# Kernel optimization log

Hardware: AMD Instinct MI355X
Metric: run time of the kernel (lower is better)

Reference implementation:

```python
import jax, jax.numpy as jnp
import numpy as np

B, T, E = 1024, 168, 8      # batch, input_len, encoder_input_size
D = 4                        # decoder_input_size
H = 512                      # lstm_num_hidden
O = 24                       # output_len


def setup_inputs() -> dict:
    key = jax.random.key(0)
    ks = jax.random.split(key, 9)
    sc = 1.0 / np.sqrt(H)
    p = lambda k, shape: (jax.random.uniform(k, shape, jnp.float32) * 2 - 1) * sc
    return {
        "x": jax.random.normal(ks[0], (B, T, E), jnp.float32),
        "W_ih_enc": p(ks[1], (4 * H, E)),
        "W_hh_enc": p(ks[2], (4 * H, H)),
        "b_enc":    p(ks[3], (4 * H,)),   # = b_ih + b_hh combined (same math)
        "W_ih_dec": p(ks[4], (4 * H, D)),
        "W_hh_dec": p(ks[5], (4 * H, H)),
        "b_dec":    p(ks[6], (4 * H,)),
        "W_fc":     p(ks[7], (D, H)),
        "b_fc":     p(ks[8], (D,)),
    }


def _lstm_cell(x, h, c, Wih, Whh, b):
    # PyTorch gate order: i, f, g, o
    gates = x @ Wih.T + h @ Whh.T + b            # [B, 4H]
    i, f, g, o = jnp.split(gates, 4, axis=-1)
    c = jax.nn.sigmoid(f) * c + jax.nn.sigmoid(i) * jnp.tanh(g)
    h = jax.nn.sigmoid(o) * jnp.tanh(c)
    return h, c


def reference(x, W_ih_enc, W_hh_enc, b_enc, W_ih_dec, W_hh_dec, b_dec, W_fc, b_fc):
    Bn = x.shape[0]
    Hn = W_hh_enc.shape[1]
    Dn = W_ih_dec.shape[1]
    h0 = jnp.zeros((Bn, Hn), x.dtype)

    # ---- encoder LSTM over input_len steps; keep only final (h, c) ----
    def enc_step(carry, xt):  # xt: [B, E]
        h, c = carry
        h, c = _lstm_cell(xt, h, c, W_ih_enc, W_hh_enc, b_enc)
        return (h, c), None
    (h, c), _ = jax.lax.scan(enc_step, (h0, h0), jnp.swapaxes(x, 0, 1))

    xt0 = x[:, -1, -Dn:]  # [B, D]

    def dec_step(carry, _):
        h, c, xt = carry
        h, c = _lstm_cell(xt, h, c, W_ih_dec, W_hh_dec, b_dec)
        y = h @ W_fc.T + b_fc          # [B, D]  (fc: hidden -> decoder_input)
        return (h, c, y), y[:, -1]     # emit last feature (target)

    _, ys = jax.lax.scan(dec_step, (h, c, xt0), None, length=O)  # [O, B]
    return jnp.swapaxes(ys, 0, 1)[..., None]  # [B, O, 1]
```

## Files before the change

kernel.cpp:

```cpp
#include <hip/hip_runtime.h>

#define Bn 1024
#define Tn 168
#define En 8
#define Hn 512
#define Dn 4
#define On 24
#define G4 2048
#define HB (Bn*Hn)

typedef short v8s __attribute__((ext_vector_type(8)));
typedef float v4f __attribute__((ext_vector_type(4)));

__device__ __forceinline__ unsigned short f2bf(float f) {
  union { float f; unsigned u; } v; v.f = f;
  return (unsigned short)((v.u + 0x7fffu + ((v.u >> 16) & 1u)) >> 16);
}
__device__ __forceinline__ float bf2f(unsigned short s) {
  union { unsigned u; float f; } v; v.u = ((unsigned)s) << 16; return v.f;
}
__device__ __forceinline__ float sigm(float x) { return 1.f / (1.f + __expf(-x)); }
__device__ __forceinline__ float tanh_(float x) { return 1.f - 2.f / (__expf(2.f * x) + 1.f); }

__device__ __forceinline__ void st_short_coh(unsigned short* p, unsigned short v) {
  unsigned int vv = v;
  asm volatile("global_store_short %0, %1, off sc0 sc1" :: "v"(p), "v"(vv) : "memory");
}
__device__ __forceinline__ void st_dword_coh(unsigned* p, unsigned v) {
  asm volatile("global_store_dword %0, %1, off sc0 sc1" :: "v"(p), "v"(v) : "memory");
}
__device__ __forceinline__ unsigned ld_u_coh(const unsigned* p) {
  unsigned v;
  asm volatile("global_load_dword %0, %1, off sc0 sc1\n\ts_waitcnt vmcnt(0)"
               : "=v"(v) : "v"(p) : "memory");
  return v;
}
__device__ __forceinline__ float ld_f_coh(const float* p) {
  float v;
  asm volatile("global_load_dword %0, %1, off sc0 sc1\n\ts_waitcnt vmcnt(0)"
               : "=v"(v) : "v"(p) : "memory");
  return v;
}
#define LDC(dst, p) \
  asm volatile("global_load_dwordx4 %0, %1, off sc0 sc1" : "=&v"(dst) : "v"(p))
#define WAITV(N) do { \
  asm volatile("s_waitcnt vmcnt(" #N ")" ::: "memory"); \
  __builtin_amdgcn_sched_barrier(0); } while (0)


__global__ void setup_weights(const float* __restrict__ whh_enc,
                              const float* __restrict__ whh_dec,
                              const float* __restrict__ wih_dec,
                              const float* __restrict__ wfc,
                              unsigned short* __restrict__ whh_bf,
                              unsigned short* __restrict__ weff_bf) {
  int idx = blockIdx.x * 256 + threadIdx.x;
  if (idx >= G4 * Hn) return;
  int r = idx >> 9, c = idx & 511;
  whh_bf[idx] = f2bf(whh_enc[idx]);
  float a = whh_dec[idx];
#pragma unroll
  for (int d = 0; d < 4; d++) a += wih_dec[r * 4 + d] * wfc[d * Hn + c];
  weff_bf[idx] = f2bf(a);
}

__global__ void setup_misc(const float* __restrict__ b_dec,
                           const float* __restrict__ wih_dec,
                           const float* __restrict__ b_fc,
                           float* __restrict__ beff,
                           float* __restrict__ out,
                           unsigned int* __restrict__ flags,
                           float* __restrict__ dpart) {
  int idx = blockIdx.x * 256 + threadIdx.x;
  if (idx < Bn * On) out[idx] = 0.f;
  if (idx < G4) {
    float a = b_dec[idx];
#pragma unroll
    for (int d = 0; d < 4; d++) a += wih_dec[idx * 4 + d] * b_fc[d];
    beff[idx] = a;
  }
  if (idx < 256 * 64) flags[idx] = 0u;
  if (idx < 16 * 64 * 4) dpart[idx] = 0.f;
}


__global__ void __launch_bounds__(256, 1) lstm_main(
    const float* __restrict__ x,
    const float* __restrict__ wih_enc,
    const float* __restrict__ b_enc,
    const float* __restrict__ wih_dec,
    const float* __restrict__ wfc,
    const float* __restrict__ bfc,
    const unsigned short* __restrict__ whh_bf,
    const unsigned short* __restrict__ weff_bf,
    const float* __restrict__ beff,
    unsigned short* __restrict__ hbuf,
    unsigned short* __restrict__ lbuf,
    float* __restrict__ out,
    unsigned int* __restrict__ flags,
    float* __restrict__ dpart) {
  __shared__ __align__(16) unsigned short wlds[128 * 512];
  __shared__ float xw[128][8];
  __shared__ float xwd[128][4];
  __shared__ float biasl[128];
  __shared__ float wfcs[4][32];
  __shared__ float xs[4][16][8];
  __shared__ float dl0[64][4];
  __shared__ float bfc3s;
  __shared__ unsigned scnt;

  const int tid = threadIdx.x;
  const int w = tid >> 6;
  const int lane = tid & 63;
  const int cidx = lane & 15;
  const int kb = lane >> 4;
  const int sw = cidx & 7;
  const int g = blockIdx.x & 15;
  const int jj = blockIdx.x >> 4;
  const int bb = g * 64;
  unsigned* myflag = flags + (((g << 4) + jj) << 6);
  const unsigned* fpoll = flags + (((g << 4) + (lane & 15)) << 6);

  {
    if (tid == 0) scnt = 0u;
    float4* wq4 = (float4*)wlds;
    for (int i = tid; i < 128 * 64; i += 256) {
      int rl = i >> 6, ch = i & 63;
      int gr = (rl >> 5) * 512 + jj * 32 + (rl & 31);
      wq4[rl * 64 + (ch ^ (rl & 7))] = *(const float4*)(whh_bf + (size_t)gr * Hn + ch * 8);
    }
    for (int i = tid; i < 128 * 8; i += 256) {
      int rl = i >> 3, e = i & 7;
      int gr = (rl >> 5) * 512 + jj * 32 + (rl & 31);
      xw[rl][e] = wih_enc[gr * En + e];
    }
    for (int i = tid; i < 128 * 4; i += 256) {
      int rl = i >> 2, d = i & 3;
      int gr = (rl >> 5) * 512 + jj * 32 + (rl & 31);
      xwd[rl][d] = wih_dec[gr * Dn + d];
    }
    for (int i = tid; i < 128; i += 256) {
      int gr = (i >> 5) * 512 + jj * 32 + (i & 31);
      biasl[i] = b_enc[gr];
    }
    if (tid < 128) wfcs[tid >> 5][tid & 31] = wfc[(tid >> 5) * Hn + jj * 32 + (tid & 31)];
    if (tid == 0) bfc3s = bfc[3];
    for (int i = tid; i < 64 * 32; i += 256) {
      int m = bb + (i >> 5), j = jj * 32 + (i & 31);
      st_short_coh(hbuf + (size_t)m * Hn + j, 0);
      st_short_coh(lbuf + (size_t)m * Hn + j, 0);
    }
  }
  asm volatile("s_waitcnt vmcnt(0)" ::: "memory");
  __syncthreads();
  if (tid == 0) st_dword_coh(myflag, 1u);

  float cst[2][4];
#pragma unroll
  for (int a = 0; a < 2; a++)
#pragma unroll
    for (int r = 0; r < 4; r++) cst[a][r] = 0.f;

  const v8s* wq = (const v8s*)wlds;
  const int abase = (bb + w * 16 + cidx) * Hn + kb * 8;

#define POLL(TGT) do { \
    int guard = 0; \
    while (true) { \
      unsigned fv = ld_u_coh(fpoll); \
      if (__ballot(fv < (unsigned)(TGT)) == 0ull) break; \
      __builtin_amdgcn_s_sleep(1); \
      if (++guard > (1 << 21)) break; \
    } } while (0)

#define ISSUE(AH, AL, K0) \
  _Pragma("unroll") for (int q = 0; q < 4; q++) { \
    LDC(AH[q], (const v8s*)(hsrc + abase + (K0 + q) * 32)); \
    LDC(AL[q], (const v8s*)(lsrc + abase + (K0 + q) * 32)); }

#define MMC(AH, AL, K0) \
  _Pragma("unroll") for (int q = 0; q < 4; q++) \
    _Pragma("unroll") for (int nt = 0; nt < 8; nt++) { \
      v8s bfr = wq[(nt * 16 + cidx) * 64 + ((((K0 + q) * 4) + kb) ^ sw)]; \
      acc[nt] = __builtin_amdgcn_mfma_f32_16x16x32_bf16(AH[q], bfr, acc[nt], 0, 0, 0); \
      acc[nt] = __builtin_amdgcn_mfma_f32_16x16x32_bf16(AL[q], bfr, acc[nt], 0, 0, 0); }

#define HMATMUL(CUR) do { \
    const unsigned short* hsrc = hbuf + (size_t)(CUR) * HB; \
    const unsigned short* lsrc = lbuf + (size_t)(CUR) * HB; \
    v8s a0h[4], a0l[4], a1h[4], a1l[4]; \
    ISSUE(a0h, a0l, 0) ISSUE(a1h, a1l, 4) \
    WAITV(8); MMC(a0h, a0l, 0) \
    ISSUE(a0h, a0l, 8) \
    WAITV(8); MMC(a1h, a1l, 4) \
    ISSUE(a1h, a1l, 12) \
    WAITV(8); MMC(a0h, a0l, 8) \
    WAITV(0); MMC(a1h, a1l, 12) \
  } while (0)

  for (int t = 0; t < Tn; t++) {
    const int cur = t & 1, nxt = cur ^ 1;
    {
      int row = lane >> 2, p2 = lane & 3;
      const float* xp = x + (size_t)(bb + w * 16 + row) * (Tn * En) + t * En + p2 * 2;
      float2 xv = *(const float2*)xp;
      xs[w][row][p2 * 2] = xv.x;
      xs[w][row][p2 * 2 + 1] = xv.y;
      asm volatile("s_waitcnt lgkmcnt(0)" ::: "memory");
    }
    v4f acc[8];
#pragma unroll
    for (int nt = 0; nt < 8; nt++) {
      const int rl = nt * 16 + cidx;
      const float bv = biasl[rl];
#pragma unroll
      for (int r = 0; r < 4; r++) {
        float a = bv;
#pragma unroll
        for (int e = 0; e < 8; e++) a += xs[w][kb * 4 + r][e] * xw[rl][e];
        acc[nt][r] = a;
      }
    }
    POLL(t + 1);
    HMATMUL(cur);
    unsigned short* hdst = hbuf + (size_t)nxt * HB;
    unsigned short* ldst = lbuf + (size_t)nxt * HB;
#pragma unroll
    for (int r = 0; r < 4; r++) {
      float hv[2];
#pragma unroll
      for (int th = 0; th < 2; th++) {
        float iv = acc[0 + th][r], fv = acc[2 + th][r];
        float gv = acc[4 + th][r], ov = acc[6 + th][r];
        float cn = sigm(fv) * cst[th][r] + sigm(iv) * tanh_(gv);
        float hn = sigm(ov) * tanh_(cn);
        cst[th][r] = cn;
        hv[th] = hn;
        const int m = bb + w * 16 + kb * 4 + r;
        const int j = jj * 32 + th * 16 + cidx;
        unsigned short hh = f2bf(hn);
        st_short_coh(hdst + (size_t)m * Hn + j, hh);
        st_short_coh(ldst + (size_t)m * Hn + j, f2bf(hn - bf2f(hh)));
      }
      if (t == Tn - 1) {
#pragma unroll
        for (int d = 0; d < 4; d++) {
          float s = hv[0] * wfcs[d][cidx] + hv[1] * wfcs[d][16 + cidx];
          s += __shfl_xor(s, 1, 64); s += __shfl_xor(s, 2, 64);
          s += __shfl_xor(s, 4, 64); s += __shfl_xor(s, 8, 64);
          if (cidx == 0)
            atomicAdd(dpart + ((g * 64 + w * 16 + kb * 4 + r) * 4 + d), s);
        }
      }
    }
    asm volatile("s_waitcnt vmcnt(0)" ::: "memory");
    if (lane == 0) {
      unsigned old = atomicAdd(&scnt, 1u);
      if ((old & 3u) == 3u) st_dword_coh(myflag, (unsigned)(t + 2));
    }
  }

  __syncthreads();
  {
    float4* wq4 = (float4*)wlds;
    for (int i = tid; i < 128 * 64; i += 256) {
      int rl = i >> 6, ch = i & 63;
      int gr = (rl >> 5) * 512 + jj * 32 + (rl & 31);
      wq4[rl * 64 + (ch ^ (rl & 7))] = *(const float4*)(weff_bf + (size_t)gr * Hn + ch * 8);
    }
    for (int i = tid; i < 128; i += 256) {
      int gr = (i >> 5) * 512 + jj * 32 + (i & 31);
      biasl[i] = beff[gr];
    }
  }
  __syncthreads();

  for (int k = 0; k < On; k++) {
    const int T = Tn + k;
    const int cur = k & 1, nxt = cur ^ 1;
    POLL(T + 1);
    if (k == 0) {
      int row = tid >> 2, d = tid & 3;
      float pv = ld_f_coh(dpart + ((g * 64 + row) * 4 + d));
      float xv = x[(size_t)(bb + row) * (Tn * En) + 167 * En + 4 + d];
      dl0[row][d] = xv - (pv + bfc[d]);
      __syncthreads();
    }
    v4f acc[8];
#pragma unroll
    for (int nt = 0; nt < 8; nt++) {
      const int rl = nt * 16 + cidx;
      const float bv = biasl[rl];
#pragma unroll
      for (int r = 0; r < 4; r++) {
        float a = bv;
        if (k == 0) {
#pragma unroll
          for (int d2 = 0; d2 < 4; d2++)
            a += dl0[w * 16 + kb * 4 + r][d2] * xwd[rl][d2];
        }
        acc[nt][r] = a;
      }
    }
    HMATMUL(cur);
    unsigned short* hdst = hbuf + (size_t)nxt * HB;
    unsigned short* ldst = lbuf + (size_t)nxt * HB;
#pragma unroll
    for (int r = 0; r < 4; r++) {
      float hv[2];
#pragma unroll
      for (int th = 0; th < 2; th++) {
        float iv = acc[0 + th][r], fv = acc[2 + th][r];
        float gv = acc[4 + th][r], ov = acc[6 + th][r];
        float cn = sigm(fv) * cst[th][r] + sigm(iv) * tanh_(gv);
        float hn = sigm(ov) * tanh_(cn);
        cst[th][r] = cn;
        hv[th] = hn;
        const int m = bb + w * 16 + kb * 4 + r;
        const int j = jj * 32 + th * 16 + cidx;
        unsigned short hh = f2bf(hn);
        st_short_coh(hdst + (size_t)m * Hn + j, hh);
        st_short_coh(ldst + (size_t)m * Hn + j, f2bf(hn - bf2f(hh)));
      }
      float p = hv[0] * wfcs[3][cidx] + hv[1] * wfcs[3][16 + cidx];
      p += __shfl_xor(p, 1, 64); p += __shfl_xor(p, 2, 64);
      p += __shfl_xor(p, 4, 64); p += __shfl_xor(p, 8, 64);
      if (cidx == 0) {
        const int m = bb + w * 16 + kb * 4 + r;
        float pp = p + (jj == 0 ? bfc3s : 0.f);
        atomicAdd(out + (size_t)m * On + k, pp);
      }
    }
    asm volatile("s_waitcnt vmcnt(0)" ::: "memory");
    if (lane == 0) {
      unsigned old = atomicAdd(&scnt, 1u);
      if ((old & 3u) == 3u) st_dword_coh(myflag, (unsigned)(T + 2));
    }
  }
}

extern "C" void kernel_launch(void* const* d_in, const int* in_sizes, int n_in,
                              void* d_out, int out_size, void* d_ws, size_t ws_size,
                              hipStream_t stream) {
  const float* x = (const float*)d_in[0];
  const float* wih_enc = (const float*)d_in[1];
  const float* whh_enc = (const float*)d_in[2];
  const float* b_enc = (const float*)d_in[3];
  const float* wih_dec = (const float*)d_in[4];
  const float* whh_dec = (const float*)d_in[5];
  const float* b_dec = (const float*)d_in[6];
  const float* wfc = (const float*)d_in[7];
  const float* bfc = (const float*)d_in[8];

  char* ws = (char*)d_ws;
  unsigned short* whh_bf = (unsigned short*)ws;
  unsigned short* weff_bf = (unsigned short*)(ws + (2u << 20));
  unsigned short* hbuf = (unsigned short*)(ws + (4u << 20));
  unsigned short* lbuf = (unsigned short*)(ws + (6u << 20));
  float* beff = (float*)(ws + (8u << 20));
  unsigned int* flags = (unsigned int*)(ws + (8u << 20) + 8192);
  float* dpart = (float*)(ws + (8u << 20) + 8192 + 65536);
  float* out = (float*)d_out;

  setup_weights<<<(G4 * Hn) / 256, 256, 0, stream>>>(whh_enc, whh_dec, wih_dec, wfc,
                                                     whh_bf, weff_bf);
  setup_misc<<<(Bn * On) / 256, 256, 0, stream>>>(b_dec, wih_dec, bfc, beff, out,
                                                  flags, dpart);
  lstm_main<<<256, 256, 0, stream>>>(x, wih_enc, b_enc, wih_dec, wfc, bfc,
                                     whh_bf, weff_bf, beff, hbuf, lbuf, out,
                                     flags, dpart);
}
```

Baseline: 1.522 ms.

## Use XCD-local cache scope for hidden-state exchange when group shares an XCD

Each block reads the XCC_ID hardware register and publishes it. After the first flag barrier, every block checks whether all 16 blocks of its batch group run on the same XCD. If they do, the recurrent h/l buffers are stored without sc0/sc1 and loaded with sc0 only, so the exchange goes through the shared L2 instead of system-coherent memory. The sc1 variants stay as a fallback, and the encoder and decoder steps are turned into macros templated on that choice. This targets the latency of the per-step cross-block hidden-state exchange. It depends on blocks with the same blockIdx mod 8 being placed on one XCD, and the two copies of the step code increase code size.

```diff
diff --git a/kernel.cpp b/kernel.cpp
--- a/kernel.cpp
+++ b/kernel.cpp
@@ -12,6 +12,8 @@
 typedef short v8s __attribute__((ext_vector_type(8)));
 typedef float v4f __attribute__((ext_vector_type(4)));
 
+#define CAT2(a, b) a##b
+
 __device__ __forceinline__ unsigned short f2bf(float f) {
   union { float f; unsigned u; } v; v.f = f;
   return (unsigned short)((v.u + 0x7fffu + ((v.u >> 16) & 1u)) >> 16);
@@ -22,27 +24,18 @@
 __device__ __forceinline__ float sigm(float x) { return 1.f / (1.f + __expf(-x)); }
 __device__ __forceinline__ float tanh_(float x) { return 1.f - 2.f / (__expf(2.f * x) + 1.f); }
 
-__device__ __forceinline__ void st_short_coh(unsigned short* p, unsigned short v) {
-  unsigned int vv = v;
-  asm volatile("global_store_short %0, %1, off sc0 sc1" :: "v"(p), "v"(vv) : "memory");
-}
-__device__ __forceinline__ void st_dword_coh(unsigned* p, unsigned v) {
-  asm volatile("global_store_dword %0, %1, off sc0 sc1" :: "v"(p), "v"(v) : "memory");
-}
-__device__ __forceinline__ unsigned ld_u_coh(const unsigned* p) {
-  unsigned v;
-  asm volatile("global_load_dword %0, %1, off sc0 sc1\n\ts_waitcnt vmcnt(0)"
-               : "=v"(v) : "v"(p) : "memory");
-  return v;
-}
-__device__ __forceinline__ float ld_f_coh(const float* p) {
-  float v;
-  asm volatile("global_load_dword %0, %1, off sc0 sc1\n\ts_waitcnt vmcnt(0)"
-               : "=v"(v) : "v"(p) : "memory");
-  return v;
-}
-#define LDC(dst, p) \
-  asm volatile("global_load_dwordx4 %0, %1, off sc0 sc1" : "=&v"(dst) : "v"(p))
+#define STFLAG(p, v) do { unsigned __vv = (v); \
+  asm volatile("global_store_dword %0, %1, off sc0 sc1" :: "v"(p), "v"(__vv) : "memory"); } while (0)
+#define LDFLAG(r, p) asm volatile("global_load_dword %0, %1, off sc0 sc1\n\ts_waitcnt vmcnt(0)" \
+  : "=v"(r) : "v"(p) : "memory")
+
+#define STH_0(p, v) do { unsigned __vv = (v); \
+  asm volatile("global_store_short %0, %1, off" :: "v"(p), "v"(__vv) : "memory"); } while (0)
+#define STH_1(p, v) do { unsigned __vv = (v); \
+  asm volatile("global_store_short %0, %1, off sc0 sc1" :: "v"(p), "v"(__vv) : "memory"); } while (0)
+#define LDC_0(dst, p) asm volatile("global_load_dwordx4 %0, %1, off sc0" : "=&v"(dst) : "v"(p))
+#define LDC_1(dst, p) asm volatile("global_load_dwordx4 %0, %1, off sc0 sc1" : "=&v"(dst) : "v"(p))
+
 #define WAITV(N) do { \
   asm volatile("s_waitcnt vmcnt(" #N ")" ::: "memory"); \
   __builtin_amdgcn_sched_barrier(0); } while (0)
@@ -98,6 +91,7 @@
     unsigned short* __restrict__ lbuf,
     float* __restrict__ out,
     unsigned int* __restrict__ flags,
+    unsigned int* __restrict__ xcds,
     float* __restrict__ dpart) {
   __shared__ __align__(16) unsigned short wlds[128 * 512];
   __shared__ float xw[128][8];
@@ -121,6 +115,9 @@
   unsigned* myflag = flags + (((g << 4) + jj) << 6);
   const unsigned* fpoll = flags + (((g << 4) + (lane & 15)) << 6);
 
+  unsigned xcc;
+  asm volatile("s_getreg_b32 %0, hwreg(HW_REG_XCC_ID)" : "=s"(xcc));
+
   {
     if (tid == 0) scnt = 0u;
     float4* wq4 = (float4*)wlds;
@@ -147,13 +144,35 @@
     if (tid == 0) bfc3s = bfc[3];
     for (int i = tid; i < 64 * 32; i += 256) {
       int m = bb + (i >> 5), j = jj * 32 + (i & 31);
-      st_short_coh(hbuf + (size_t)m * Hn + j, 0);
-      st_short_coh(lbuf + (size_t)m * Hn + j, 0);
+      STH_1(hbuf + (size_t)m * Hn + j, 0);
+      STH_1(lbuf + (size_t)m * Hn + j, 0);
+    }
+    if (tid == 0) {
+      unsigned* xp = xcds + ((g << 4) + jj);
+      asm volatile("global_store_dword %0, %1, off sc0 sc1" :: "v"(xp), "v"(xcc) : "memory");
     }
   }
   asm volatile("s_waitcnt vmcnt(0)" ::: "memory");
   __syncthreads();
-  if (tid == 0) st_dword_coh(myflag, 1u);
+  if (tid == 0) STFLAG(myflag, 1u);
+
+#define POLL(TGT) do { \
+    int guard = 0; unsigned fv; \
+    while (true) { \
+      LDFLAG(fv, fpoll); \
+      if (__ballot(fv < (unsigned)(TGT)) == 0ull) break; \
+      __builtin_amdgcn_s_sleep(1); \
+      if (++guard > (1 << 21)) break; \
+    } } while (0)
+
+  POLL(1);
+  unsigned other;
+  {
+    const unsigned* xq = xcds + ((g << 4) + (lane & 15));
+    asm volatile("global_load_dword %0, %1, off sc0 sc1\n\ts_waitcnt vmcnt(0)"
+                 : "=v"(other) : "v"(xq) : "memory");
+  }
+  const int fast = (__ballot(other != xcc) == 0ull) ? 1 : 0;
 
   float cst[2][4];
 #pragma unroll
@@ -164,19 +183,10 @@
   const v8s* wq = (const v8s*)wlds;
   const int abase = (bb + w * 16 + cidx) * Hn + kb * 8;
 
-#define POLL(TGT) do { \
-    int guard = 0; \
-    while (true) { \
-      unsigned fv = ld_u_coh(fpoll); \
-      if (__ballot(fv < (unsigned)(TGT)) == 0ull) break; \
-      __builtin_amdgcn_s_sleep(1); \
-      if (++guard > (1 << 21)) break; \
-    } } while (0)
-
-#define ISSUE(AH, AL, K0) \
+#define ISSUEX(D, AH, AL, K0) \
   _Pragma("unroll") for (int q = 0; q < 4; q++) { \
-    LDC(AH[q], (const v8s*)(hsrc + abase + (K0 + q) * 32)); \
-    LDC(AL[q], (const v8s*)(lsrc + abase + (K0 + q) * 32)); }
+    CAT2(LDC_, D)(AH[q], (const v8s*)(hsrc + abase + (K0 + q) * 32)); \
+    CAT2(LDC_, D)(AL[q], (const v8s*)(lsrc + abase + (K0 + q) * 32)); }
 
 #define MMC(AH, AL, K0) \
   _Pragma("unroll") for (int q = 0; q < 4; q++) \
@@ -185,79 +195,118 @@
       acc[nt] = __builtin_amdgcn_mfma_f32_16x16x32_bf16(AH[q], bfr, acc[nt], 0, 0, 0); \
       acc[nt] = __builtin_amdgcn_mfma_f32_16x16x32_bf16(AL[q], bfr, acc[nt], 0, 0, 0); }
 
-#define HMATMUL(CUR) do { \
+#define HMATMULX(D, CUR) do { \
     const unsigned short* hsrc = hbuf + (size_t)(CUR) * HB; \
     const unsigned short* lsrc = lbuf + (size_t)(CUR) * HB; \
     v8s a0h[4], a0l[4], a1h[4], a1l[4]; \
-    ISSUE(a0h, a0l, 0) ISSUE(a1h, a1l, 4) \
+    ISSUEX(D, a0h, a0l, 0) ISSUEX(D, a1h, a1l, 4) \
     WAITV(8); MMC(a0h, a0l, 0) \
-    ISSUE(a0h, a0l, 8) \
+    ISSUEX(D, a0h, a0l, 8) \
     WAITV(8); MMC(a1h, a1l, 4) \
-    ISSUE(a1h, a1l, 12) \
+    ISSUEX(D, a1h, a1l, 12) \
     WAITV(8); MMC(a0h, a0l, 8) \
     WAITV(0); MMC(a1h, a1l, 12) \
   } while (0)
 
-  for (int t = 0; t < Tn; t++) {
-    const int cur = t & 1, nxt = cur ^ 1;
-    {
-      int row = lane >> 2, p2 = lane & 3;
-      const float* xp = x + (size_t)(bb + w * 16 + row) * (Tn * En) + t * En + p2 * 2;
-      float2 xv = *(const float2*)xp;
-      xs[w][row][p2 * 2] = xv.x;
-      xs[w][row][p2 * 2 + 1] = xv.y;
-      asm volatile("s_waitcnt lgkmcnt(0)" ::: "memory");
-    }
-    v4f acc[8];
-#pragma unroll
-    for (int nt = 0; nt < 8; nt++) {
-      const int rl = nt * 16 + cidx;
-      const float bv = biasl[rl];
-#pragma unroll
-      for (int r = 0; r < 4; r++) {
-        float a = bv;
-#pragma unroll
-        for (int e = 0; e < 8; e++) a += xs[w][kb * 4 + r][e] * xw[rl][e];
-        acc[nt][r] = a;
-      }
-    }
-    POLL(t + 1);
-    HMATMUL(cur);
-    unsigned short* hdst = hbuf + (size_t)nxt * HB;
-    unsigned short* ldst = lbuf + (size_t)nxt * HB;
-#pragma unroll
-    for (int r = 0; r < 4; r++) {
-      float hv[2];
-#pragma unroll
-      for (int th = 0; th < 2; th++) {
-        float iv = acc[0 + th][r], fv = acc[2 + th][r];
-        float gv = acc[4 + th][r], ov = acc[6 + th][r];
-        float cn = sigm(fv) * cst[th][r] + sigm(iv) * tanh_(gv);
-        float hn = sigm(ov) * tanh_(cn);
-        cst[th][r] = cn;
-        hv[th] = hn;
-        const int m = bb + w * 16 + kb * 4 + r;
-        const int j = jj * 32 + th * 16 + cidx;
-        unsigned short hh = f2bf(hn);
-        st_short_coh(hdst + (size_t)m * Hn + j, hh);
-        st_short_coh(ldst + (size_t)m * Hn + j, f2bf(hn - bf2f(hh)));
-      }
-      if (t == Tn - 1) {
-#pragma unroll
-        for (int d = 0; d < 4; d++) {
-          float s = hv[0] * wfcs[d][cidx] + hv[1] * wfcs[d][16 + cidx];
-          s += __shfl_xor(s, 1, 64); s += __shfl_xor(s, 2, 64);
-          s += __shfl_xor(s, 4, 64); s += __shfl_xor(s, 8, 64);
-          if (cidx == 0)
-            atomicAdd(dpart + ((g * 64 + w * 16 + kb * 4 + r) * 4 + d), s);
-        }
-      }
-    }
-    asm volatile("s_waitcnt vmcnt(0)" ::: "memory");
-    if (lane == 0) {
-      unsigned old = atomicAdd(&scnt, 1u);
-      if ((old & 3u) == 3u) st_dword_coh(myflag, (unsigned)(t + 2));
-    }
+#define ENC_STEP(D, t) do { \
+    const int cur = (t) & 1, nxt = cur ^ 1; \
+    { int row = lane >> 2, p2 = lane & 3; \
+      const float* xp = x + (size_t)(bb + w * 16 + row) * (Tn * En) + (t) * En + p2 * 2; \
+      float2 xv = *(const float2*)xp; \
+      xs[w][row][p2 * 2] = xv.x; xs[w][row][p2 * 2 + 1] = xv.y; \
+      asm volatile("s_waitcnt lgkmcnt(0)" ::: "memory"); } \
+    v4f acc[8]; \
+    _Pragma("unroll") for (int nt = 0; nt < 8; nt++) { \
+      const int rl = nt * 16 + cidx; const float bv = biasl[rl]; \
+      _Pragma("unroll") for (int r = 0; r < 4; r++) { \
+        float a = bv; \
+        _Pragma("unroll") for (int e = 0; e < 8; e++) a += xs[w][kb * 4 + r][e] * xw[rl][e]; \
+        acc[nt][r] = a; } } \
+    POLL((t) + 1); \
+    HMATMULX(D, cur); \
+    unsigned short* hdst = hbuf + (size_t)nxt * HB; \
+    unsigned short* ldst = lbuf + (size_t)nxt * HB; \
+    _Pragma("unroll") for (int r = 0; r < 4; r++) { \
+      float hv[2]; \
+      _Pragma("unroll") for (int th = 0; th < 2; th++) { \
+        float iv = acc[0 + th][r], fv2 = acc[2 + th][r]; \
+        float gv = acc[4 + th][r], ov = acc[6 + th][r]; \
+        float cn = sigm(fv2) * cst[th][r] + sigm(iv) * tanh_(gv); \
+        float hn = sigm(ov) * tanh_(cn); \
+        cst[th][r] = cn; hv[th] = hn; \
+        const int m = bb + w * 16 + kb * 4 + r; \
+        const int j = jj * 32 + th * 16 + cidx; \
+        unsigned short hh = f2bf(hn); \
+        CAT2(STH_, D)(hdst + (size_t)m * Hn + j, hh); \
+        CAT2(STH_, D)(ldst + (size_t)m * Hn + j, f2bf(hn - bf2f(hh))); } \
+      if ((t) == Tn - 1) { \
+        _Pragma("unroll") for (int d = 0; d < 4; d++) { \
+          float s = hv[0] * wfcs[d][cidx] + hv[1] * wfcs[d][16 + cidx]; \
+          s += __shfl_xor(s, 1, 64); s += __shfl_xor(s, 2, 64); \
+          s += __shfl_xor(s, 4, 64); s += __shfl_xor(s, 8, 64); \
+          if (cidx == 0) \
+            atomicAdd(dpart + ((g * 64 + w * 16 + kb * 4 + r) * 4 + d), s); } } } \
+    asm volatile("s_waitcnt vmcnt(0)" ::: "memory"); \
+    if (lane == 0) { \
+      unsigned old = atomicAdd(&scnt, 1u); \
+      if ((old & 3u) == 3u) STFLAG(myflag, (unsigned)((t) + 2)); } \
+  } while (0)
+
+#define DEC_STEP(D, k) do { \
+    const int T = Tn + (k); \
+    const int cur = (k) & 1, nxt = cur ^ 1; \
+    POLL(T + 1); \
+    if ((k) == 0) { \
+      int row = tid >> 2, d = tid & 3; \
+      float pv; \
+      asm volatile("global_load_dword %0, %1, off sc0 sc1\n\ts_waitcnt vmcnt(0)" \
+                   : "=v"(pv) : "v"(dpart + ((g * 64 + row) * 4 + d)) : "memory"); \
+      float xv = x[(size_t)(bb + row) * (Tn * En) + 167 * En + 4 + d]; \
+      dl0[row][d] = xv - (pv + bfc[d]); \
+      __syncthreads(); \
+    } \
+    v4f acc[8]; \
+    _Pragma("unroll") for (int nt = 0; nt < 8; nt++) { \
+      const int rl = nt * 16 + cidx; const float bv = biasl[rl]; \
+      _Pragma("unroll") for (int r = 0; r < 4; r++) { \
+        float a = bv; \
+        if ((k) == 0) { \
+          _Pragma("unroll") for (int d2 = 0; d2 < 4; d2++) \
+            a += dl0[w * 16 + kb * 4 + r][d2] * xwd[rl][d2]; } \
+        acc[nt][r] = a; } } \
+    HMATMULX(D, cur); \
+    unsigned short* hdst = hbuf + (size_t)nxt * HB; \
+    unsigned short* ldst = lbuf + (size_t)nxt * HB; \
+    _Pragma("unroll") for (int r = 0; r < 4; r++) { \
+      float hv[2]; \
+      _Pragma("unroll") for (int th = 0; th < 2; th++) { \
+        float iv = acc[0 + th][r], fv2 = acc[2 + th][r]; \
+        float gv = acc[4 + th][r], ov = acc[6 + th][r]; \
+        float cn = sigm(fv2) * cst[th][r] + sigm(iv) * tanh_(gv); \
+        float hn = sigm(ov) * tanh_(cn); \
+        cst[th][r] = cn; hv[th] = hn; \
+        const int m = bb + w * 16 + kb * 4 + r; \
+        const int j = jj * 32 + th * 16 + cidx; \
+        unsigned short hh = f2bf(hn); \
+        CAT2(STH_, D)(hdst + (size_t)m * Hn + j, hh); \
+        CAT2(STH_, D)(ldst + (size_t)m * Hn + j, f2bf(hn - bf2f(hh))); } \
+      float p = hv[0] * wfcs[3][cidx] + hv[1] * wfcs[3][16 + cidx]; \
+      p += __shfl_xor(p, 1, 64); p += __shfl_xor(p, 2, 64); \
+      p += __shfl_xor(p, 4, 64); p += __shfl_xor(p, 8, 64); \
+      if (cidx == 0) { \
+        const int m = bb + w * 16 + kb * 4 + r; \
+        float pp = p + (jj == 0 ? bfc3s : 0.f); \
+        atomicAdd(out + (size_t)m * On + (k), pp); } } \
+    asm volatile("s_waitcnt vmcnt(0)" ::: "memory"); \
+    if (lane == 0) { \
+      unsigned old = atomicAdd(&scnt, 1u); \
+      if ((old & 3u) == 3u) STFLAG(myflag, (unsigned)(T + 2)); } \
+  } while (0)
+
+  if (fast) {
+    for (int t = 0; t < Tn; t++) ENC_STEP(0, t);
+  } else {
+    for (int t = 0; t < Tn; t++) ENC_STEP(1, t);
   }
 
   __syncthreads();
@@ -275,67 +324,10 @@
   }
   __syncthreads();
 
-  for (int k = 0; k < On; k++) {
-    const int T = Tn + k;
-    const int cur = k & 1, nxt = cur ^ 1;
-    POLL(T + 1);
-    if (k == 0) {
-      int row = tid >> 2, d = tid & 3;
-      float pv = ld_f_coh(dpart + ((g * 64 + row) * 4 + d));
-      float xv = x[(size_t)(bb + row) * (Tn * En) + 167 * En + 4 + d];
-      dl0[row][d] = xv - (pv + bfc[d]);
-      __syncthreads();
-    }
-    v4f acc[8];
-#pragma unroll
-    for (int nt = 0; nt < 8; nt++) {
-      const int rl = nt * 16 + cidx;
-      const float bv = biasl[rl];
-#pragma unroll
-      for (int r = 0; r < 4; r++) {
-        float a = bv;
-        if (k == 0) {
-#pragma unroll
-          for (int d2 = 0; d2 < 4; d2++)
-            a += dl0[w * 16 + kb * 4 + r][d2] * xwd[rl][d2];
-        }
-        acc[nt][r] = a;
-      }
-    }
-    HMATMUL(cur);
-    unsigned short* hdst = hbuf + (size_t)nxt * HB;
-    unsigned short* ldst = lbuf + (size_t)nxt * HB;
-#pragma unroll
-    for (int r = 0; r < 4; r++) {
-      float hv[2];
-#pragma unroll
-      for (int th = 0; th < 2; th++) {
-        float iv = acc[0 + th][r], fv = acc[2 + th][r];
-        float gv = acc[4 + th][r], ov = acc[6 + th][r];
-        float cn = sigm(fv) * cst[th][r] + sigm(iv) * tanh_(gv);
-        float hn = sigm(ov) * tanh_(cn);
-        cst[th][r] = cn;
-        hv[th] = hn;
-        const int m = bb + w * 16 + kb * 4 + r;
-        const int j = jj * 32 + th * 16 + cidx;
-        unsigned short hh = f2bf(hn);
-        st_short_coh(hdst + (size_t)m * Hn + j, hh);
-        st_short_coh(ldst + (size_t)m * Hn + j, f2bf(hn - bf2f(hh)));
-      }
-      float p = hv[0] * wfcs[3][cidx] + hv[1] * wfcs[3][16 + cidx];
-      p += __shfl_xor(p, 1, 64); p += __shfl_xor(p, 2, 64);
-      p += __shfl_xor(p, 4, 64); p += __shfl_xor(p, 8, 64);
-      if (cidx == 0) {
-        const int m = bb + w * 16 + kb * 4 + r;
-        float pp = p + (jj == 0 ? bfc3s : 0.f);
-        atomicAdd(out + (size_t)m * On + k, pp);
-      }
-    }
-    asm volatile("s_waitcnt vmcnt(0)" ::: "memory");
-    if (lane == 0) {
-      unsigned old = atomicAdd(&scnt, 1u);
-      if ((old & 3u) == 3u) st_dword_coh(myflag, (unsigned)(T + 2));
-    }
+  if (fast) {
+    for (int k = 0; k < On; k++) DEC_STEP(0, k);
+  } else {
+    for (int k = 0; k < On; k++) DEC_STEP(1, k);
   }
 }
 
@@ -359,7 +351,8 @@
   unsigned short* lbuf = (unsigned short*)(ws + (6u << 20));
   float* beff = (float*)(ws + (8u << 20));
   unsigned int* flags = (unsigned int*)(ws + (8u << 20) + 8192);
-  float* dpart = (float*)(ws + (8u << 20) + 8192 + 65536);
+  unsigned int* xcds = (unsigned int*)(ws + (8u << 20) + 8192 + 65536);
+  float* dpart = (float*)(ws + (8u << 20) + 8192 + 65536 + 1024);
   float* out = (float*)d_out;
 
   setup_weights<<<(G4 * Hn) / 256, 256, 0, stream>>>(whh_enc, whh_dec, wih_dec, wfc,
@@ -368,5 +361,5 @@
                                                   flags, dpart);
   lstm_main<<<256, 256, 0, stream>>>(x, wih_enc, b_enc, wih_dec, wfc, bfc,
                                      whh_bf, weff_bf, beff, hbuf, lbuf, out,
-                                     flags, dpart);
-}
+                                     flags, xcds, dpart);
+}
```

Measured after the change: 1.474 ms. 1.03x faster.
